# Kernel tuning notes

Measured on AMD Instinct MI355X. Metric: run time of the kernel, lower is better.

The kernel has to match this reference:

```python
import jax, jax.numpy as jnp
import numpy as np

N = 50000      # nodes
E = 800000     # edges (before self-loops)
IN_F = 64
HID = 96
OUT_F = 16
L = 16         # num GCN2Conv layers
ALPHA = 0.1
THETA = 0.5


def setup_inputs() -> dict:
    key = jax.random.key(0)
    ks = jax.random.split(key, 6)
    x = jax.random.normal(ks[0], (N, IN_F), jnp.float32)
    edge_index = jax.random.randint(ks[1], (2, E), 0, N, jnp.int64)
    lin0_w = jax.random.normal(ks[2], (HID, IN_F), jnp.float32) * 0.05
    lin0_b = jnp.zeros((HID,), jnp.float32)
    lin1_w = jax.random.normal(ks[3], (OUT_F, HID), jnp.float32) * 0.05
    lin1_b = jnp.zeros((OUT_F,), jnp.float32)
    conv_w = jax.random.normal(ks[4], (L, HID, HID), jnp.float32) * 0.05
    return {"x": x, "edge_index": edge_index, "lin0_w": lin0_w, "lin0_b": lin0_b,
            "lin1_w": lin1_w, "lin1_b": lin1_b, "conv_w": conv_w}


def _gcn_norm(edge_index, n):
    # add self-loops, symmetric normalization D^-1/2 A D^-1/2 (edge weights = 1)
    loops = jnp.arange(n, dtype=edge_index.dtype)
    row = jnp.concatenate([edge_index[0], loops])
    col = jnp.concatenate([edge_index[1], loops])
    ones = jnp.ones(row.shape[0], jnp.float32)
    deg = jax.ops.segment_sum(ones, col, num_segments=n)
    dis = jnp.where(deg > 0, jax.lax.rsqrt(deg), 0.0)
    val = dis[row] * dis[col]
    return row, col, val


def reference(x, edge_index, lin0_w, lin0_b, lin1_w, lin1_b, conv_w):
    n = x.shape[0]
    row, col, val = _gcn_norm(edge_index, n)
    h = jax.nn.relu(x @ lin0_w.T + lin0_b)            # [N, HID]
    x0 = h
    betas = jnp.log(THETA / jnp.arange(1.0, L + 1.0) + 1.0).astype(jnp.float32)

    def layer(h, wb):
        w, beta = wb
        # SpMM: out[i] = sum_{(i,j) in E} val * h[j]
        m = jax.ops.segment_sum(val[:, None] * h[col], row, num_segments=n)
        s = (1.0 - ALPHA) * m + ALPHA * x0            # initial-residual combine
        out = (1.0 - beta) * s + beta * (s @ w)       # identity mapping (shared weights)
        return jax.nn.relu(out), None

    h, _ = jax.lax.scan(layer, h, (conv_w, betas))
    return h @ lin1_w.T + lin1_b
```

## Files before the change

kernel.cpp:

```cpp
#include <hip/hip_runtime.h>

#define NTHREADS 256
#define HID 96
#define INF 64
#define OUTF 16
#define NLAYERS 16
#define NHW 25088
#define CB 64

typedef __attribute__((ext_vector_type(8))) unsigned short ushort8_t;
typedef __attribute__((ext_vector_type(8))) short short8_t;
typedef __attribute__((ext_vector_type(4))) float f32x4_t;

static __device__ __forceinline__ float bf2f(unsigned short u) {
  return __uint_as_float(((unsigned)u) << 16);
}
static __device__ __forceinline__ unsigned short f2bf(float x) {
  unsigned u = __float_as_uint(x);
  return (unsigned short)((u + 0x7FFF + ((u >> 16) & 1)) >> 16);
}
static __device__ __forceinline__ unsigned pack2bf(float a, float b) {
  return (unsigned)f2bf(a) | ((unsigned)f2bf(b) << 16);
}

__global__ __launch_bounds__(NTHREADS) void k_hist(
    const int* __restrict__ idx, int e, unsigned* __restrict__ part, int nw) {
  __shared__ unsigned hh[NHW];
  int tid = threadIdx.x;
  for (int i = tid; i < NHW; i += NTHREADS) hh[i] = 0;
  __syncthreads();
  int per = (e + CB - 1) / CB;
  int s = blockIdx.x * per;
  int en = min(e, s + per);
  for (int i = s + tid; i < en; i += NTHREADS) {
    int v = idx[i];
    atomicAdd(&hh[v >> 1], (v & 1) ? 0x10000u : 1u);
  }
  __syncthreads();
  unsigned* dst = part + (size_t)blockIdx.x * NHW;
  for (int i = tid; i < nw; i += NTHREADS) dst[i] = hh[i];
}

__global__ void k_hmerge(unsigned* __restrict__ partR,
                         const unsigned* __restrict__ partC,
                         int* __restrict__ cnt, int* __restrict__ deg,
                         int n, int nw) {
  int w = blockIdx.x * NTHREADS + threadIdx.x;
  if (w >= nw) return;
  unsigned rl = 0, rh = 0, cl = 0, ch = 0;
  for (int b = 0; b < CB; ++b) {
    size_t o = (size_t)b * NHW + w;
    unsigned pr = partR[o];
    partR[o] = rl | (rh << 16);
    rl += pr & 0xFFFFu; rh += pr >> 16;
    unsigned pc = partC[o];
    cl += pc & 0xFFFFu; ch += pc >> 16;
  }
  int i0 = 2 * w, i1 = 2 * w + 1;
  if (i0 < n) { cnt[i0] = 1 + (int)rl; deg[i0] = 1 + (int)cl; }
  if (i1 < n) { cnt[i1] = 1 + (int)rh; deg[i1] = 1 + (int)ch; }
}

__global__ void k_dis(const int* __restrict__ deg, float* __restrict__ dis,
                      float* __restrict__ selfval, int n) {
  int i = blockIdx.x * NTHREADS + threadIdx.x;
  if (i < n) {
    float d = (float)deg[i];
    dis[i] = rsqrtf(d);
    selfval[i] = 1.0f / d;
  }
}

__global__ void k_scan1(const int* __restrict__ cnt, int* __restrict__ rp,
                        int* __restrict__ bsum, int n) {
  __shared__ int sh[NTHREADS];
  int t = threadIdx.x;
  int i = blockIdx.x * NTHREADS + t;
  int v = (i < n) ? cnt[i] : 0;
  sh[t] = v;
  __syncthreads();
  for (int ofs = 1; ofs < NTHREADS; ofs <<= 1) {
    int u = (t >= ofs) ? sh[t - ofs] : 0;
    __syncthreads();
    sh[t] += u;
    __syncthreads();
  }
  if (i < n) rp[i] = sh[t] - v;
  if (t == NTHREADS - 1) bsum[blockIdx.x] = sh[t];
}

__global__ void k_scan2(int* __restrict__ bsum, int nb) {
  __shared__ int sh[NTHREADS];
  int t = threadIdx.x;
  int v = (t < nb) ? bsum[t] : 0;
  sh[t] = v;
  __syncthreads();
  for (int ofs = 1; ofs < NTHREADS; ofs <<= 1) {
    int u = (t >= ofs) ? sh[t - ofs] : 0;
    __syncthreads();
    sh[t] += u;
    __syncthreads();
  }
  if (t < nb) bsum[t] = sh[t] - v;
}

__global__ void k_scan3(int* __restrict__ rp, const int* __restrict__ bsum,
                        int n, int etot) {
  int i = blockIdx.x * NTHREADS + threadIdx.x;
  if (i < n) rp[i] += bsum[blockIdx.x];
  if (i == 0) rp[n] = etot;
}

__global__ void k_self(const int* __restrict__ rp, const float* __restrict__ sv,
                       int2* __restrict__ ev, int n) {
  int i = blockIdx.x * NTHREADS + threadIdx.x;
  if (i < n) {
    int2 v;
    v.x = i;
    v.y = __float_as_int(sv[i]);
    ev[rp[i]] = v;
  }
}

__global__ __launch_bounds__(NTHREADS) void k_scatter2(
    const int* __restrict__ row, const int* __restrict__ col,
    const int* __restrict__ rp, const unsigned* __restrict__ prefR,
    const float* __restrict__ dis, int2* __restrict__ ev, int e) {
  __shared__ unsigned lcur[NHW];
  int tid = threadIdx.x;
  for (int i = tid; i < NHW; i += NTHREADS) lcur[i] = 0;
  __syncthreads();
  int per = (e + CB - 1) / CB;
  int s = blockIdx.x * per;
  int en = min(e, s + per);
  const unsigned* pref = prefR + (size_t)blockIdx.x * NHW;
  for (int i = s + tid; i < en; i += NTHREADS) {
    int r = row[i], c = col[i];
    unsigned old = atomicAdd(&lcur[r >> 1], (r & 1) ? 0x10000u : 1u);
    unsigned loc = (r & 1) ? (old >> 16) : (old & 0xFFFFu);
    unsigned pw = pref[r >> 1];
    unsigned pb = (r & 1) ? (pw >> 16) : (pw & 0xFFFFu);
    int p = rp[r] + 1 + (int)pb + (int)loc;
    int2 v;
    v.x = c;
    v.y = __float_as_int(dis[r] * dis[c]);
    ev[p] = v;
  }
}

__global__ void k_wprime(const float* __restrict__ cw,
                         unsigned short* __restrict__ wTb) {
  int l = blockIdx.y;
  int idx = blockIdx.x * NTHREADS + threadIdx.x;
  int f = idx / HID, k = idx % HID;
  wTb[l * HID * HID + idx] = f2bf(cw[l * HID * HID + k * HID + f]);
}

__global__ __launch_bounds__(NTHREADS) void k_lin0(
    const float* __restrict__ x, const float* __restrict__ w0,
    const float* __restrict__ b0, unsigned short* __restrict__ x0b, int n) {
  __shared__ float wl[INF * HID];
  __shared__ float xT[INF * 68];
  int tid = threadIdx.x;
#pragma unroll
  for (int i = 0; i < 6; ++i) {
    int idx = tid + i * NTHREADS;
    int hrow = idx / 16, q = idx % 16;
    float4 v = *(const float4*)(w0 + hrow * INF + q * 4);
    wl[(q * 4 + 0) * HID + hrow] = v.x;
    wl[(q * 4 + 1) * HID + hrow] = v.y;
    wl[(q * 4 + 2) * HID + hrow] = v.z;
    wl[(q * 4 + 3) * HID + hrow] = v.w;
  }
  int r0 = blockIdx.x * 64;
#pragma unroll
  for (int i = 0; i < 4; ++i) {
    int idx = tid + i * NTHREADS;
    int r = idx / 16, q = idx % 16;
    int gr = r0 + r;
    float4 v = make_float4(0.f, 0.f, 0.f, 0.f);
    if (gr < n) v = *(const float4*)(x + (size_t)gr * INF + q * 4);
    xT[(q * 4 + 0) * 68 + r] = v.x;
    xT[(q * 4 + 1) * 68 + r] = v.y;
    xT[(q * 4 + 2) * 68 + r] = v.z;
    xT[(q * 4 + 3) * 68 + r] = v.w;
  }
  __syncthreads();
  int rg = tid & 15, cg = tid >> 4;
  float acc[4][6];
#pragma unroll
  for (int i = 0; i < 4; ++i)
#pragma unroll
    for (int j = 0; j < 6; ++j) acc[i][j] = 0.f;
#pragma unroll 4
  for (int k = 0; k < INF; ++k) {
    float4 s4 = *(const float4*)(xT + k * 68 + rg * 4);
    const float2* w2 = (const float2*)(wl + k * HID + cg * 6);
    float2 wa = w2[0], wb = w2[1], wc = w2[2];
    float wv[6] = {wa.x, wa.y, wb.x, wb.y, wc.x, wc.y};
    float sv[4] = {s4.x, s4.y, s4.z, s4.w};
#pragma unroll
    for (int i = 0; i < 4; ++i)
#pragma unroll
      for (int j = 0; j < 6; ++j) acc[i][j] = fmaf(sv[i], wv[j], acc[i][j]);
  }
  float bb[6];
#pragma unroll
  for (int j = 0; j < 6; ++j) bb[j] = b0[cg * 6 + j];
#pragma unroll
  for (int i = 0; i < 4; ++i) {
    int gr = r0 + rg * 4 + i;
    if (gr < n) {
      float r_[6];
#pragma unroll
      for (int j = 0; j < 6; ++j) r_[j] = fmaxf(acc[i][j] + bb[j], 0.f);
      unsigned* ob = (unsigned*)(x0b + (size_t)gr * HID + cg * 6);
      ob[0] = pack2bf(r_[0], r_[1]);
      ob[1] = pack2bf(r_[2], r_[3]);
      ob[2] = pack2bf(r_[4], r_[5]);
    }
  }
}

__global__ __launch_bounds__(NTHREADS) void k_spmm(
    const unsigned short* __restrict__ hin, const unsigned short* __restrict__ x0,
    unsigned short* __restrict__ sout, const int* __restrict__ rp,
    const int2* __restrict__ ev, int n) {
  __shared__ float red[8][8][100];
  int t = threadIdx.x;
  int hw = t >> 5;
  int lane = t & 31;
  int eb = lane >> 2;
  int fg = lane & 3;
  int r = blockIdx.x * 8 + hw;
  if (r >= n) r = n - 1;
  int e0 = rp[r], e1 = rp[r + 1];
  float acc[24];
#pragma unroll
  for (int j = 0; j < 24; ++j) acc[j] = 0.f;

  int idx0 = e0 + eb;
  bool ok = idx0 < e1;
  idx0 = ok ? idx0 : e1 - 1;
  int2 cv = ev[idx0];
  for (int base = e0; base < e1; base += 8) {
    int2 cur = cv;
    bool okc = ok;
    int nb = base + 8;
    if (nb < e1) {
      int i2 = nb + eb;
      ok = i2 < e1;
      i2 = ok ? i2 : e1 - 1;
      cv = ev[i2];
    }
    float v = okc ? __int_as_float(cur.y) : 0.f;
    const unsigned short* hc = hin + (size_t)cur.x * HID + fg * 24;
    ushort8_t p0 = *(const ushort8_t*)(hc);
    ushort8_t p1 = *(const ushort8_t*)(hc + 8);
    ushort8_t p2 = *(const ushort8_t*)(hc + 16);
#pragma unroll
    for (int j = 0; j < 8; ++j) acc[j]      = fmaf(v, bf2f(p0[j]), acc[j]);
#pragma unroll
    for (int j = 0; j < 8; ++j) acc[8 + j]  = fmaf(v, bf2f(p1[j]), acc[8 + j]);
#pragma unroll
    for (int j = 0; j < 8; ++j) acc[16 + j] = fmaf(v, bf2f(p2[j]), acc[16 + j]);
  }
  float* myr = &red[hw][eb][fg * 24];
#pragma unroll
  for (int j = 0; j < 6; ++j)
    *(float4*)(myr + j * 4) =
        make_float4(acc[j * 4], acc[j * 4 + 1], acc[j * 4 + 2], acc[j * 4 + 3]);
  asm volatile("s_waitcnt lgkmcnt(0)" ::: "memory");
  __builtin_amdgcn_wave_barrier();
  if (lane < 24) {
    float4 tot = *(const float4*)(&red[hw][0][lane * 4]);
#pragma unroll
    for (int b = 1; b < 8; ++b) {
      float4 p = *(const float4*)(&red[hw][b][lane * 4]);
      tot.x += p.x; tot.y += p.y; tot.z += p.z; tot.w += p.w;
    }
    size_t o = (size_t)r * HID + lane * 4;
    const unsigned* xr = (const unsigned*)(x0 + o);
    unsigned xa = xr[0], xb = xr[1];
    float s0 = 0.9f * tot.x + 0.1f * bf2f((unsigned short)(xa & 0xFFFFu));
    float s1 = 0.9f * tot.y + 0.1f * bf2f((unsigned short)(xa >> 16));
    float s2 = 0.9f * tot.z + 0.1f * bf2f((unsigned short)(xb & 0xFFFFu));
    float s3 = 0.9f * tot.w + 0.1f * bf2f((unsigned short)(xb >> 16));
    unsigned* op = (unsigned*)(sout + o);
    op[0] = pack2bf(s0, s1);
    op[1] = pack2bf(s2, s3);
  }
}

__global__ __launch_bounds__(NTHREADS) void k_gemm(
    const unsigned short* __restrict__ s, const unsigned short* __restrict__ wT,
    unsigned short* __restrict__ hout, float omb, float beta, int n) {
  __shared__ unsigned short sT[64 * 104];
  __shared__ unsigned short wl[HID * 104];
  int tid = threadIdx.x;
  int r0 = blockIdx.x * 64;
#pragma unroll
  for (int i = 0; i < 3; ++i) {
    int idx = tid + i * NTHREADS;
    int r = idx / 12, q = idx % 12;
    int gr = r0 + r;
    ushort8_t v = (ushort8_t)0;
    if (gr < n) v = *(const ushort8_t*)(s + (size_t)gr * HID + q * 8);
    *(ushort8_t*)(sT + r * 104 + q * 8) = v;
  }
#pragma unroll
  for (int i = 0; i < 5; ++i) {
    int idx = tid + i * NTHREADS;
    if (idx < 1152) {
      int f = idx / 12, c = (idx % 12) * 8;
      ushort8_t v = *(const ushort8_t*)(wT + f * HID + c);
      *(ushort8_t*)(wl + f * 104 + c) = v;
    }
  }
  __syncthreads();
  int lane = tid & 63, wave = tid >> 6;
  int l15 = lane & 15;
  int kg = lane >> 4;
  f32x4_t acc[6];
#pragma unroll
  for (int i = 0; i < 6; ++i) acc[i] = (f32x4_t)(0.f);
#pragma unroll
  for (int kt = 0; kt < 3; ++kt) {
    short8_t A = *(const short8_t*)(sT + (wave * 16 + l15) * 104 + kt * 32 + kg * 8);
#pragma unroll
    for (int ft = 0; ft < 6; ++ft) {
      short8_t B = *(const short8_t*)(wl + (ft * 16 + l15) * 104 + kt * 32 + kg * 8);
      acc[ft] = __builtin_amdgcn_mfma_f32_16x16x32_bf16(A, B, acc[ft], 0, 0, 0);
    }
  }
#pragma unroll
  for (int ft = 0; ft < 6; ++ft) {
    int col = ft * 16 + l15;
#pragma unroll
    for (int j = 0; j < 4; ++j) {
      int rl = wave * 16 + kg * 4 + j;
      int gr = r0 + rl;
      float sv = bf2f(sT[rl * 104 + col]);
      float o = fmaxf(omb * sv + beta * acc[ft][j], 0.f);
      if (gr < n) hout[(size_t)gr * HID + col] = f2bf(o);
    }
  }
}

__global__ __launch_bounds__(NTHREADS) void k_lin1(
    const unsigned short* __restrict__ h, const float* __restrict__ w1,
    const float* __restrict__ b1, float* __restrict__ out, int n) {
  __shared__ float hT[HID * 68];
  __shared__ float w1l[HID * OUTF];
  int tid = threadIdx.x;
#pragma unroll
  for (int i = 0; i < 6; ++i) {
    int idx = tid + i * NTHREADS;
    int o = idx / HID, k = idx % HID;
    w1l[k * OUTF + o] = w1[idx];
  }
  int r0 = blockIdx.x * 64;
#pragma unroll
  for (int i = 0; i < 3; ++i) {
    int idx = tid + i * NTHREADS;
    int r = idx / 12, q = idx % 12;
    int gr = r0 + r;
    ushort8_t v = (ushort8_t)0;
    if (gr < n) v = *(const ushort8_t*)(h + (size_t)gr * HID + q * 8);
#pragma unroll
    for (int j = 0; j < 8; ++j) hT[(q * 8 + j) * 68 + r] = bf2f(v[j]);
  }
  __syncthreads();
  int r = tid & 63, og = tid >> 6;
  float acc[4] = {0.f, 0.f, 0.f, 0.f};
#pragma unroll 4
  for (int k = 0; k < HID; ++k) {
    float s = hT[k * 68 + r];
    float4 w4 = *(const float4*)(w1l + k * OUTF + og * 4);
    acc[0] = fmaf(s, w4.x, acc[0]);
    acc[1] = fmaf(s, w4.y, acc[1]);
    acc[2] = fmaf(s, w4.z, acc[2]);
    acc[3] = fmaf(s, w4.w, acc[3]);
  }
  int gr = r0 + r;
  if (gr < n) {
    float* op = out + (size_t)gr * OUTF + og * 4;
#pragma unroll
    for (int j = 0; j < 4; ++j) op[j] = acc[j] + b1[og * 4 + j];
  }
}

extern "C" void kernel_launch(void* const* d_in, const int* in_sizes, int n_in,
                              void* d_out, int out_size, void* d_ws, size_t ws_size,
                              hipStream_t stream) {
  const float* x  = (const float*)d_in[0];
  const int*   ei = (const int*)d_in[1];
  const float* w0 = (const float*)d_in[2];
  const float* b0 = (const float*)d_in[3];
  const float* w1 = (const float*)d_in[4];
  const float* b1 = (const float*)d_in[5];
  const float* cw = (const float*)d_in[6];
  int n = in_sizes[0] / INF;
  int e = in_sizes[1] / 2;
  const int* row = ei;
  const int* col = ei + e;

  char* ws = (char*)d_ws;
  size_t off = 0;
  auto alloc = [&](size_t bytes) -> void* {
    void* p = (void*)(ws + off);
    off += (bytes + 255) & ~(size_t)255;
    return p;
  };
  unsigned short* x0b = (unsigned short*)alloc((size_t)n * HID * 2);
  unsigned short* sb  = (unsigned short*)alloc((size_t)n * HID * 2);
  unsigned short* hbA = (unsigned short*)alloc((size_t)n * HID * 2);
  unsigned short* hbB = (unsigned short*)alloc((size_t)n * HID * 2);
  unsigned short* wTb = (unsigned short*)alloc((size_t)NLAYERS * HID * HID * 2);
  int*   deg  = (int*)alloc((size_t)n * 4);
  float* dis  = (float*)alloc((size_t)n * 4);
  float* sv   = (float*)alloc((size_t)n * 4);
  int*   cnt  = (int*)alloc((size_t)n * 4);
  int*   rp   = (int*)alloc((size_t)(n + 1) * 4);
  int2*  ev   = (int2*)alloc((size_t)(e + n) * 8);
  int*   bsum = (int*)alloc(1024 * 4);
  unsigned* partR = (unsigned*)alloc((size_t)CB * NHW * 4);
  unsigned* partC = (unsigned*)alloc((size_t)CB * NHW * 4);
  int nw = (n + 1) / 2;
  (void)ws_size; (void)n_in; (void)out_size;

  int nb  = (n + NTHREADS - 1) / NTHREADS;
  int r64 = (n + 63) / 64;

  k_hist<<<CB, NTHREADS, 0, stream>>>(row, e, partR, nw);
  k_hist<<<CB, NTHREADS, 0, stream>>>(col, e, partC, nw);
  k_hmerge<<<(nw + NTHREADS - 1) / NTHREADS, NTHREADS, 0, stream>>>(
      partR, partC, cnt, deg, n, nw);
  k_dis<<<nb, NTHREADS, 0, stream>>>(deg, dis, sv, n);
  k_scan1<<<nb, NTHREADS, 0, stream>>>(cnt, rp, bsum, n);
  k_scan2<<<1, NTHREADS, 0, stream>>>(bsum, nb);
  k_scan3<<<nb, NTHREADS, 0, stream>>>(rp, bsum, n, e + n);
  k_self<<<nb, NTHREADS, 0, stream>>>(rp, sv, ev, n);
  k_scatter2<<<CB, NTHREADS, 0, stream>>>(row, col, rp, partR, dis, ev, e);
  k_wprime<<<dim3(36, NLAYERS), NTHREADS, 0, stream>>>(cw, wTb);
  k_lin0<<<r64, NTHREADS, 0, stream>>>(x, w0, b0, x0b, n);

  const unsigned short* hin = x0b;
  for (int l = 0; l < NLAYERS; ++l) {
    unsigned short* hout = (l & 1) ? hbB : hbA;
    float beta = logf(0.5f / (float)(l + 1) + 1.0f);
    k_spmm<<<(n + 7) / 8, NTHREADS, 0, stream>>>(hin, x0b, sb, rp, ev, n);
    k_gemm<<<r64, NTHREADS, 0, stream>>>(sb, wTb + (size_t)l * HID * HID,
                                         hout, 1.0f - beta, beta, n);
    hin = hout;
  }
  k_lin1<<<r64, NTHREADS, 0, stream>>>(hin, w1, b1, (float*)d_out, n);
}
```

Before: 694.9 us.

## Fuse SpMM and dense GEMM into one per-layer kernel via shared memory

Each GCN layer's SpMM and GEMM become one kernel, k_layer. Each block gathers and reduces 64 rows, writes the combined s tile into shared memory, then runs the MFMA GEMM on it. This removes the global round trip of the intermediate s buffer and one launch per layer. The cost is 8x fewer blocks, each looping serially over 8 row groups, which cuts the parallelism available to hide gather latency. Separately, the histogram uses 128 partition blocks instead of 64, and the partition buffers now alias the x0b, hbA and hbB workspace.

```diff
diff --git a/kernel.cpp b/kernel.cpp
--- a/kernel.cpp
+++ b/kernel.cpp
@@ -6,7 +6,7 @@
 #define OUTF 16
 #define NLAYERS 16
 #define NHW 25088
-#define CB 64
+#define CB 128
 
 typedef __attribute__((ext_vector_type(8))) unsigned short ushort8_t;
 typedef __attribute__((ext_vector_type(8))) short short8_t;
@@ -48,6 +48,7 @@
   int w = blockIdx.x * NTHREADS + threadIdx.x;
   if (w >= nw) return;
   unsigned rl = 0, rh = 0, cl = 0, ch = 0;
+#pragma unroll 4
   for (int b = 0; b < CB; ++b) {
     size_t o = (size_t)b * NHW + w;
     unsigned pr = partR[o];
@@ -222,115 +223,105 @@
   }
 }
 
-__global__ __launch_bounds__(NTHREADS) void k_spmm(
+__global__ __launch_bounds__(NTHREADS) void k_layer(
     const unsigned short* __restrict__ hin, const unsigned short* __restrict__ x0,
-    unsigned short* __restrict__ sout, const int* __restrict__ rp,
-    const int2* __restrict__ ev, int n) {
-  __shared__ float red[8][8][100];
-  int t = threadIdx.x;
-  int hw = t >> 5;
-  int lane = t & 31;
-  int eb = lane >> 2;
-  int fg = lane & 3;
-  int r = blockIdx.x * 8 + hw;
-  if (r >= n) r = n - 1;
-  int e0 = rp[r], e1 = rp[r + 1];
-  float acc[24];
-#pragma unroll
-  for (int j = 0; j < 24; ++j) acc[j] = 0.f;
-
-  int idx0 = e0 + eb;
-  bool ok = idx0 < e1;
-  idx0 = ok ? idx0 : e1 - 1;
-  int2 cv = ev[idx0];
-  for (int base = e0; base < e1; base += 8) {
-    int2 cur = cv;
-    bool okc = ok;
-    int nb = base + 8;
-    if (nb < e1) {
-      int i2 = nb + eb;
-      ok = i2 < e1;
-      i2 = ok ? i2 : e1 - 1;
-      cv = ev[i2];
-    }
-    float v = okc ? __int_as_float(cur.y) : 0.f;
-    const unsigned short* hc = hin + (size_t)cur.x * HID + fg * 24;
-    ushort8_t p0 = *(const ushort8_t*)(hc);
-    ushort8_t p1 = *(const ushort8_t*)(hc + 8);
-    ushort8_t p2 = *(const ushort8_t*)(hc + 16);
-#pragma unroll
-    for (int j = 0; j < 8; ++j) acc[j]      = fmaf(v, bf2f(p0[j]), acc[j]);
-#pragma unroll
-    for (int j = 0; j < 8; ++j) acc[8 + j]  = fmaf(v, bf2f(p1[j]), acc[8 + j]);
-#pragma unroll
-    for (int j = 0; j < 8; ++j) acc[16 + j] = fmaf(v, bf2f(p2[j]), acc[16 + j]);
-  }
-  float* myr = &red[hw][eb][fg * 24];
-#pragma unroll
-  for (int j = 0; j < 6; ++j)
-    *(float4*)(myr + j * 4) =
-        make_float4(acc[j * 4], acc[j * 4 + 1], acc[j * 4 + 2], acc[j * 4 + 3]);
-  asm volatile("s_waitcnt lgkmcnt(0)" ::: "memory");
-  __builtin_amdgcn_wave_barrier();
-  if (lane < 24) {
-    float4 tot = *(const float4*)(&red[hw][0][lane * 4]);
-#pragma unroll
-    for (int b = 1; b < 8; ++b) {
-      float4 p = *(const float4*)(&red[hw][b][lane * 4]);
-      tot.x += p.x; tot.y += p.y; tot.z += p.z; tot.w += p.w;
-    }
-    size_t o = (size_t)r * HID + lane * 4;
-    const unsigned* xr = (const unsigned*)(x0 + o);
-    unsigned xa = xr[0], xb = xr[1];
-    float s0 = 0.9f * tot.x + 0.1f * bf2f((unsigned short)(xa & 0xFFFFu));
-    float s1 = 0.9f * tot.y + 0.1f * bf2f((unsigned short)(xa >> 16));
-    float s2 = 0.9f * tot.z + 0.1f * bf2f((unsigned short)(xb & 0xFFFFu));
-    float s3 = 0.9f * tot.w + 0.1f * bf2f((unsigned short)(xb >> 16));
-    unsigned* op = (unsigned*)(sout + o);
-    op[0] = pack2bf(s0, s1);
-    op[1] = pack2bf(s2, s3);
-  }
-}
-
-__global__ __launch_bounds__(NTHREADS) void k_gemm(
-    const unsigned short* __restrict__ s, const unsigned short* __restrict__ wT,
-    unsigned short* __restrict__ hout, float omb, float beta, int n) {
-  __shared__ unsigned short sT[64 * 104];
-  __shared__ unsigned short wl[HID * 104];
+    const int* __restrict__ rp, const int2* __restrict__ ev,
+    const unsigned short* __restrict__ wT, unsigned short* __restrict__ hout,
+    float omb, float beta, int n) {
+  __shared__ unsigned char pool[38912] __attribute__((aligned(16)));
+  float* red = (float*)pool;
+  unsigned short* wl = (unsigned short*)pool;
+  unsigned short* sT = (unsigned short*)(pool + 25600);
   int tid = threadIdx.x;
+  int hw = tid >> 5, lane = tid & 31;
+  int eb = lane >> 2, fg = lane & 3;
   int r0 = blockIdx.x * 64;
-#pragma unroll
-  for (int i = 0; i < 3; ++i) {
-    int idx = tid + i * NTHREADS;
-    int r = idx / 12, q = idx % 12;
-    int gr = r0 + r;
-    ushort8_t v = (ushort8_t)0;
-    if (gr < n) v = *(const ushort8_t*)(s + (size_t)gr * HID + q * 8);
-    *(ushort8_t*)(sT + r * 104 + q * 8) = v;
-  }
+
+  for (int sub = 0; sub < 8; ++sub) {
+    int rl = sub * 8 + hw;
+    int r = r0 + rl;
+    if (r >= n) r = n - 1;
+    int e0 = rp[r], e1 = rp[r + 1];
+    float acc[24];
+#pragma unroll
+    for (int j = 0; j < 24; ++j) acc[j] = 0.f;
+    int idx0 = e0 + eb;
+    bool ok = idx0 < e1;
+    idx0 = ok ? idx0 : e1 - 1;
+    int2 cv = ev[idx0];
+    for (int base = e0; base < e1; base += 8) {
+      int2 cur = cv;
+      bool okc = ok;
+      int nb = base + 8;
+      if (nb < e1) {
+        int i2 = nb + eb;
+        ok = i2 < e1;
+        i2 = ok ? i2 : e1 - 1;
+        cv = ev[i2];
+      }
+      float v = okc ? __int_as_float(cur.y) : 0.f;
+      const unsigned short* hc = hin + (size_t)cur.x * HID + fg * 24;
+      ushort8_t p0 = *(const ushort8_t*)(hc);
+      ushort8_t p1 = *(const ushort8_t*)(hc + 8);
+      ushort8_t p2 = *(const ushort8_t*)(hc + 16);
+#pragma unroll
+      for (int j = 0; j < 8; ++j) acc[j]      = fmaf(v, bf2f(p0[j]), acc[j]);
+#pragma unroll
+      for (int j = 0; j < 8; ++j) acc[8 + j]  = fmaf(v, bf2f(p1[j]), acc[8 + j]);
+#pragma unroll
+      for (int j = 0; j < 8; ++j) acc[16 + j] = fmaf(v, bf2f(p2[j]), acc[16 + j]);
+    }
+    float* myr = red + (hw * 8 + eb) * 100 + fg * 24;
+#pragma unroll
+    for (int j = 0; j < 6; ++j)
+      *(float4*)(myr + j * 4) =
+          make_float4(acc[j * 4], acc[j * 4 + 1], acc[j * 4 + 2], acc[j * 4 + 3]);
+    asm volatile("s_waitcnt lgkmcnt(0)" ::: "memory");
+    __builtin_amdgcn_wave_barrier();
+    if (lane < 24) {
+      const float* base = red + hw * 800 + lane * 4;
+      float4 tot = *(const float4*)(base);
+#pragma unroll
+      for (int b = 1; b < 8; ++b) {
+        float4 p = *(const float4*)(base + b * 100);
+        tot.x += p.x; tot.y += p.y; tot.z += p.z; tot.w += p.w;
+      }
+      const unsigned* xr = (const unsigned*)(x0 + (size_t)r * HID + lane * 4);
+      unsigned xa = xr[0], xb = xr[1];
+      float s0 = 0.9f * tot.x + 0.1f * bf2f((unsigned short)(xa & 0xFFFFu));
+      float s1 = 0.9f * tot.y + 0.1f * bf2f((unsigned short)(xa >> 16));
+      float s2 = 0.9f * tot.z + 0.1f * bf2f((unsigned short)(xb & 0xFFFFu));
+      float s3 = 0.9f * tot.w + 0.1f * bf2f((unsigned short)(xb >> 16));
+      unsigned* op = (unsigned*)(sT + rl * 104 + lane * 4);
+      op[0] = pack2bf(s0, s1);
+      op[1] = pack2bf(s2, s3);
+    }
+    asm volatile("" ::: "memory");
+    __builtin_amdgcn_wave_barrier();
+  }
+  __syncthreads();
 #pragma unroll
   for (int i = 0; i < 5; ++i) {
     int idx = tid + i * NTHREADS;
     if (idx < 1152) {
       int f = idx / 12, c = (idx % 12) * 8;
-      ushort8_t v = *(const ushort8_t*)(wT + f * HID + c);
-      *(ushort8_t*)(wl + f * 104 + c) = v;
-    }
-  }
-  __syncthreads();
-  int lane = tid & 63, wave = tid >> 6;
-  int l15 = lane & 15;
-  int kg = lane >> 4;
-  f32x4_t acc[6];
-#pragma unroll
-  for (int i = 0; i < 6; ++i) acc[i] = (f32x4_t)(0.f);
+      *(ushort8_t*)(wl + f * 104 + c) = *(const ushort8_t*)(wT + f * HID + c);
+    }
+  }
+  __syncthreads();
+  int lane64 = tid & 63, wave = tid >> 6;
+  int l15 = lane64 & 15;
+  int kg = lane64 >> 4;
+  f32x4_t acc2[6];
+#pragma unroll
+  for (int i = 0; i < 6; ++i) acc2[i] = (f32x4_t)(0.f);
 #pragma unroll
   for (int kt = 0; kt < 3; ++kt) {
     short8_t A = *(const short8_t*)(sT + (wave * 16 + l15) * 104 + kt * 32 + kg * 8);
 #pragma unroll
     for (int ft = 0; ft < 6; ++ft) {
       short8_t B = *(const short8_t*)(wl + (ft * 16 + l15) * 104 + kt * 32 + kg * 8);
-      acc[ft] = __builtin_amdgcn_mfma_f32_16x16x32_bf16(A, B, acc[ft], 0, 0, 0);
+      acc2[ft] = __builtin_amdgcn_mfma_f32_16x16x32_bf16(A, B, acc2[ft], 0, 0, 0);
     }
   }
 #pragma unroll
@@ -341,7 +332,7 @@
       int rl = wave * 16 + kg * 4 + j;
       int gr = r0 + rl;
       float sv = bf2f(sT[rl * 104 + col]);
-      float o = fmaxf(omb * sv + beta * acc[ft][j], 0.f);
+      float o = fmaxf(omb * sv + beta * acc2[ft][j], 0.f);
       if (gr < n) hout[(size_t)gr * HID + col] = f2bf(o);
     }
   }
@@ -413,7 +404,6 @@
     return p;
   };
   unsigned short* x0b = (unsigned short*)alloc((size_t)n * HID * 2);
-  unsigned short* sb  = (unsigned short*)alloc((size_t)n * HID * 2);
   unsigned short* hbA = (unsigned short*)alloc((size_t)n * HID * 2);
   unsigned short* hbB = (unsigned short*)alloc((size_t)n * HID * 2);
   unsigned short* wTb = (unsigned short*)alloc((size_t)NLAYERS * HID * HID * 2);
@@ -424,8 +414,8 @@
   int*   rp   = (int*)alloc((size_t)(n + 1) * 4);
   int2*  ev   = (int2*)alloc((size_t)(e + n) * 8);
   int*   bsum = (int*)alloc(1024 * 4);
-  unsigned* partR = (unsigned*)alloc((size_t)CB * NHW * 4);
-  unsigned* partC = (unsigned*)alloc((size_t)CB * NHW * 4);
+  unsigned* partR = (unsigned*)x0b;
+  unsigned* partC = partR + (size_t)CB * NHW;
   int nw = (n + 1) / 2;
   (void)ws_size; (void)n_in; (void)out_size;
 
@@ -449,9 +439,9 @@
   for (int l = 0; l < NLAYERS; ++l) {
     unsigned short* hout = (l & 1) ? hbB : hbA;
     float beta = logf(0.5f / (float)(l + 1) + 1.0f);
-    k_spmm<<<(n + 7) / 8, NTHREADS, 0, stream>>>(hin, x0b, sb, rp, ev, n);
-    k_gemm<<<r64, NTHREADS, 0, stream>>>(sb, wTb + (size_t)l * HID * HID,
-                                         hout, 1.0f - beta, beta, n);
+    k_layer<<<r64, NTHREADS, 0, stream>>>(hin, x0b, rp, ev,
+                                          wTb + (size_t)l * HID * HID, hout,
+                                          1.0f - beta, beta, n);
     hin = hout;
   }
   k_lin1<<<r64, NTHREADS, 0, stream>>>(hin, w1, b1, (float*)d_out, n);
```

Result: faster. 646.6 us (-6.9%).
